# Kernel optimization log

Hardware: AMD Instinct MI355X
Metric: run time of the kernel (lower is better)

## Reference

```python
import jax, jax.numpy as jnp
import numpy as np

B, F, V, E = 4096, 26, 20000, 64
LAYERS = [256, 128, 1]


def setup_inputs() -> dict:
    key = jax.random.key(0)
    ks = jax.random.split(key, 13)
    s = 1.0 / np.sqrt(E)
    inp = {
        "x_idx": jax.random.randint(ks[0], (B, F), 0, V),
        # per-field embedding tables [F, V, E] and linear (bias) tables [F, V, 1]
        "embed_w": jax.random.normal(ks[1], (F, V, E), jnp.float32) * 0.01,
        "embed_b": jax.random.normal(ks[2], (F, V, 1), jnp.float32) * 0.01,
        "attention_w": jax.random.normal(ks[3], (E, E), jnp.float32) * s,
        "attention_b": jax.random.normal(ks[4], (1, E), jnp.float32) * 0.01,
        "attention_p": jax.random.normal(ks[5], (E,), jnp.float32) * 0.01,
        "w0": jax.random.normal(ks[6], (E, LAYERS[0]), jnp.float32) * s,
        "b0": jnp.zeros((LAYERS[0],), jnp.float32),
        "w1": jax.random.normal(ks[7], (LAYERS[0], LAYERS[1]), jnp.float32) * (1.0 / np.sqrt(LAYERS[0])),
        "b1": jnp.zeros((LAYERS[1],), jnp.float32),
        "w2": jax.random.normal(ks[8], (LAYERS[1], LAYERS[2]), jnp.float32) * (1.0 / np.sqrt(LAYERS[1])),
        "b2": jnp.zeros((LAYERS[2],), jnp.float32),
        "bias": jnp.zeros((1,), jnp.float32),
    }
    return inp


def _gather_fields(tables, idx):
    # tables: [F, V, D], idx: [B, F] -> [B, F, D]
    return jax.vmap(lambda tbl, i: tbl[i], in_axes=(0, 1), out_axes=1)(tables, idx)


def reference(x_idx, embed_w, embed_b, attention_w, attention_b, attention_p,
              w0, b0, w1, b1, w2, b2, bias):
    f = embed_w.shape[0]
    xw = _gather_fields(embed_w, x_idx)                      # [B, F, E]
    iu, ju = jnp.triu_indices(f, k=1)                        # P = F*(F-1)/2 pairs, loop order i<j
    pairs = xw[:, iu, :] * xw[:, ju, :]                      # [B, P, E] pairwise FM interactions
    # attention network: relu(pairs @ W + b), score = <p, .>, softmax over pairs
    att_h = jax.nn.relu(jnp.einsum('bpe,ef->bpf', pairs, attention_w) + attention_b)
    scores = jnp.sum(attention_p * att_h, axis=2, keepdims=True)   # [B, P, 1]
    att_out = jax.nn.softmax(scores, axis=1)                       # softmax pooling over pairs
    afm = jnp.sum(att_out * pairs, axis=1)                         # [B, E]
    # MLP head
    h = jax.nn.relu(afm @ w0 + b0)
    h = jax.nn.relu(h @ w1 + b1)
    bilinear = h @ w2 + b2                                         # [B, 1]
    # linear (LR) term from per-field bias tables
    lr = jnp.sum(_gather_fields(embed_b, x_idx), axis=1)           # [B, 1]
    return bilinear + lr + bias
```

## Files before the change

kernel.cpp:

```cpp
#include <hip/hip_runtime.h>
#include <stdint.h>

#define B_N 4096
#define F_N 26
#define V_N 20000
#define E_N 64
#define P_N 325
#define PT  21
#define SPB 8

typedef __attribute__((ext_vector_type(8))) _Float16 half8;
typedef __attribute__((ext_vector_type(4))) _Float16 half4;
typedef __attribute__((ext_vector_type(4))) float floatx4;

__global__ __launch_bounds__(512, 4) void anfm_fused_kernel(
    const int* __restrict__ x_idx, const float* __restrict__ embed_w,
    const float* __restrict__ embed_b, const float* __restrict__ att_w,
    const float* __restrict__ att_b, const float* __restrict__ att_p,
    const float* __restrict__ w0, const float* __restrict__ b0,
    const float* __restrict__ w1, const float* __restrict__ b1,
    const float* __restrict__ w2, const float* __restrict__ b2,
    const float* __restrict__ bias, float* __restrict__ out)
{
    __shared__ _Float16 xwb[SPB][F_N][72];
    __shared__ _Float16 WT[64][72];
    __shared__ unsigned short pijL[336];
    __shared__ float apL[64], abL[64];
    __shared__ _Float16 afmL[16][72];
    __shared__ _Float16 h0L[16][264];
    __shared__ float    h1L[16][132];
    __shared__ float    lrL[SPB];

    const int tid  = threadIdx.x;
    const int lane = tid & 63;
    const int wid  = tid >> 6;
    const int c16  = lane & 15;
    const int g    = lane >> 4;
    const int b    = blockIdx.x * SPB + wid;

    int myidx = (lane < F_N) ? x_idx[b * F_N + lane] : 0;
    float lv  = (lane < F_N) ? embed_b[lane * V_N + myidx] : 0.f;
    float4 gv[7];
    #pragma unroll
    for (int it = 0; it < 7; it++) {
        int f = it * 4 + g;
        int fc = (f < F_N) ? f : 0;
        int idxf = __shfl(myidx, fc);
        const float4* src = reinterpret_cast<const float4*>(
            embed_w + ((size_t)(fc * V_N + idxf)) * E_N);
        gv[it] = src[c16];
    }

    if (tid < 336) {
        int p = tid;
        int i = 0, j = 1;
        if (p < P_N) {
            i = (int)((51.0f - sqrtf(2601.0f - 8.0f * (float)p)) * 0.5f);
            if (i * (51 - i) / 2 > p) i--;
            else if ((i + 1) * (50 - i) / 2 <= p) i++;
            j = p - i * (51 - i) / 2 + i + 1;
        }
        pijL[p] = (unsigned short)((i << 8) | j);
    } else if (tid < 400) {
        apL[tid - 336] = att_p[tid - 336];
    } else if (tid < 464) {
        abL[tid - 400] = att_b[tid - 400];
    }
    for (int z = tid; z < 576; z += 512) {
        int r = z / 72, c = z - r * 72;
        afmL[8 + r][c] = (_Float16)0.f;
    }
    for (int idx = tid; idx < 64 * 64; idx += 512) {
        int k = idx >> 6, col = idx & 63;
        WT[col][k] = (_Float16)att_w[idx];
    }

    #pragma unroll
    for (int it = 0; it < 7; it++) {
        int f = it * 4 + g;
        if (f < F_N) {
            float4 v = gv[it];
            half4 hv = {(_Float16)v.x, (_Float16)v.y, (_Float16)v.z, (_Float16)v.w};
            *reinterpret_cast<half4*>(&xwb[wid][f][c16 * 4]) = hv;
        }
    }
    __syncthreads();

    half8 bfr[4][2];
    #pragma unroll
    for (int nt = 0; nt < 4; nt++)
        #pragma unroll
        for (int s = 0; s < 2; s++)
            bfr[nt][s] = *reinterpret_cast<const half8*>(
                &WT[nt * 16 + c16][s * 32 + g * 8]);

    float acf[16];
    #pragma unroll
    for (int u = 0; u < 16; u++) acf[u] = 0.f;
    float Zp = 0.f;

    #pragma unroll 1
    for (int t = 0; t < PT; t++) {
        int pk = pijL[t * 16 + c16];
        int ri = pk >> 8, rj = pk & 255;
        half8 af[2];
        #pragma unroll
        for (int s = 0; s < 2; s++) {
            half8 xv = *reinterpret_cast<const half8*>(&xwb[wid][ri][s * 32 + g * 8]);
            half8 yv = *reinterpret_cast<const half8*>(&xwb[wid][rj][s * 32 + g * 8]);
            af[s] = xv * yv;
        }
        float scq = 0.f;
        #pragma unroll
        for (int nt = 0; nt < 4; nt++) {
            floatx4 acc = *reinterpret_cast<const floatx4*>(&abL[nt * 16 + g * 4]);
            acc = __builtin_amdgcn_mfma_f32_16x16x32_f16(bfr[nt][0], af[0], acc, 0, 0, 0);
            acc = __builtin_amdgcn_mfma_f32_16x16x32_f16(bfr[nt][1], af[1], acc, 0, 0, 0);
            floatx4 ap4 = *reinterpret_cast<const floatx4*>(&apL[nt * 16 + g * 4]);
            #pragma unroll
            for (int r = 0; r < 4; r++)
                scq = fmaf(ap4[r], fmaxf(acc[r], 0.f), scq);
        }
        scq += __shfl_xor(scq, 16);
        scq += __shfl_xor(scq, 32);
        float w = (t * 16 + c16 < P_N) ? __expf(scq) : 0.f;
        Zp += w;
        #pragma unroll
        for (int s = 0; s < 2; s++)
            #pragma unroll
            for (int u = 0; u < 8; u++)
                acf[s * 8 + u] = fmaf((float)af[s][u], w, acf[s * 8 + u]);
    }

    #pragma unroll
    for (int msk = 1; msk <= 8; msk <<= 1) {
        Zp += __shfl_xor(Zp, msk);
        #pragma unroll
        for (int u = 0; u < 16; u++) acf[u] += __shfl_xor(acf[u], msk);
    }

    if (c16 == 0) {
        float rZ = 1.f / Zp;
        #pragma unroll
        for (int s = 0; s < 2; s++) {
            half4 o0 = {(_Float16)(acf[s * 8 + 0] * rZ), (_Float16)(acf[s * 8 + 1] * rZ),
                        (_Float16)(acf[s * 8 + 2] * rZ), (_Float16)(acf[s * 8 + 3] * rZ)};
            half4 o1 = {(_Float16)(acf[s * 8 + 4] * rZ), (_Float16)(acf[s * 8 + 5] * rZ),
                        (_Float16)(acf[s * 8 + 6] * rZ), (_Float16)(acf[s * 8 + 7] * rZ)};
            *reinterpret_cast<half4*>(&afmL[wid][s * 32 + g * 8])     = o0;
            *reinterpret_cast<half4*>(&afmL[wid][s * 32 + g * 8 + 4]) = o1;
        }
    }
    #pragma unroll
    for (int off = 32; off; off >>= 1) lv += __shfl_xor(lv, off);
    if (lane == 0) lrL[wid] = lv;
    __syncthreads();


    {
        half8 af0[2];
        #pragma unroll
        for (int s = 0; s < 2; s++)
            af0[s] = *reinterpret_cast<const half8*>(&afmL[c16][s * 32 + g * 8]);
        #pragma unroll
        for (int q = 0; q < 2; q++) {
            int n = (wid * 2 + q) * 16 + c16;
            half8 bf[2];
            #pragma unroll
            for (int s = 0; s < 2; s++)
                #pragma unroll
                for (int u = 0; u < 8; u++)
                    bf[s][u] = (_Float16)w0[(s * 32 + g * 8 + u) * 256 + n];
            floatx4 acc = {0.f, 0.f, 0.f, 0.f};
            acc = __builtin_amdgcn_mfma_f32_16x16x32_f16(af0[0], bf[0], acc, 0, 0, 0);
            acc = __builtin_amdgcn_mfma_f32_16x16x32_f16(af0[1], bf[1], acc, 0, 0, 0);
            float b0n = b0[n];
            #pragma unroll
            for (int r = 0; r < 4; r++)
                h0L[g * 4 + r][n] = (_Float16)fmaxf(acc[r] + b0n, 0.f);
        }
    }
    __syncthreads();

    {
        int n = wid * 16 + c16;
        floatx4 acc = {0.f, 0.f, 0.f, 0.f};
        #pragma unroll
        for (int ks = 0; ks < 8; ks++) {
            half8 af1 = *reinterpret_cast<const half8*>(&h0L[c16][ks * 32 + g * 8]);
            half8 bf;
            #pragma unroll
            for (int u = 0; u < 8; u++)
                bf[u] = (_Float16)w1[(ks * 32 + g * 8 + u) * 128 + n];
            acc = __builtin_amdgcn_mfma_f32_16x16x32_f16(af1, bf, acc, 0, 0, 0);
        }
        float b1n = b1[n];
        #pragma unroll
        for (int r = 0; r < 4; r++)
            h1L[g * 4 + r][n] = fmaxf(acc[r] + b1n, 0.f);
    }
    __syncthreads();

    {
        float part = fmaf(h1L[wid][lane * 2], w2[lane * 2],
                          h1L[wid][lane * 2 + 1] * w2[lane * 2 + 1]);
        #pragma unroll
        for (int off = 32; off; off >>= 1) part += __shfl_xor(part, off);
        if (lane == 0)
            out[blockIdx.x * SPB + wid] = part + b2[0] + bias[0] + lrL[wid];
    }
}

extern "C" void kernel_launch(void* const* d_in, const int* in_sizes, int n_in,
                              void* d_out, int out_size, void* d_ws, size_t ws_size,
                              hipStream_t stream) {
    const int*   x_idx   = (const int*)d_in[0];
    const float* embed_w = (const float*)d_in[1];
    const float* embed_b = (const float*)d_in[2];
    const float* att_w   = (const float*)d_in[3];
    const float* att_b   = (const float*)d_in[4];
    const float* att_p   = (const float*)d_in[5];
    const float* w0      = (const float*)d_in[6];
    const float* b0      = (const float*)d_in[7];
    const float* w1      = (const float*)d_in[8];
    const float* b1      = (const float*)d_in[9];
    const float* w2      = (const float*)d_in[10];
    const float* b2      = (const float*)d_in[11];
    const float* bias    = (const float*)d_in[12];
    float*       out     = (float*)d_out;

    anfm_fused_kernel<<<B_N / SPB, 512, 0, stream>>>(
        x_idx, embed_w, embed_b, att_w, att_b, att_p,
        w0, b0, w1, b1, w2, b2, bias, out);
}
```

Baseline: 34.28 us.

## Split each sample's pair loop across two waves, halving samples per block

```diff
diff --git a/kernel.cpp b/kernel.cpp
--- a/kernel.cpp
+++ b/kernel.cpp
@@ -7,7 +7,7 @@
 #define E_N 64
 #define P_N 325
 #define PT  21
-#define SPB 8
+#define SPB 4
 
 typedef __attribute__((ext_vector_type(8))) _Float16 half8;
 typedef __attribute__((ext_vector_type(4))) _Float16 half4;
@@ -26,24 +26,28 @@
     __shared__ _Float16 WT[64][72];
     __shared__ unsigned short pijL[336];
     __shared__ float apL[64], abL[64];
+    __shared__ float afm_part[SPB][2][64];
+    __shared__ float ZpL[SPB][2];
+    __shared__ float lrL[SPB];
     __shared__ _Float16 afmL[16][72];
     __shared__ _Float16 h0L[16][264];
     __shared__ float    h1L[16][132];
-    __shared__ float    lrL[SPB];
 
     const int tid  = threadIdx.x;
     const int lane = tid & 63;
     const int wid  = tid >> 6;
     const int c16  = lane & 15;
     const int g    = lane >> 4;
-    const int b    = blockIdx.x * SPB + wid;
+    const int smp  = wid >> 1;
+    const int wv   = wid & 1;
+    const int b    = blockIdx.x * SPB + smp;
 
     int myidx = (lane < F_N) ? x_idx[b * F_N + lane] : 0;
-    float lv  = (lane < F_N) ? embed_b[lane * V_N + myidx] : 0.f;
-    float4 gv[7];
-    #pragma unroll
-    for (int it = 0; it < 7; it++) {
-        int f = it * 4 + g;
+    float lv  = (wv == 0 && lane < F_N) ? embed_b[lane * V_N + myidx] : 0.f;
+    float4 gv[4];
+    #pragma unroll
+    for (int it = 0; it < 4; it++) {
+        int f = it * 8 + wv * 4 + g;
         int fc = (f < F_N) ? f : 0;
         int idxf = __shfl(myidx, fc);
         const float4* src = reinterpret_cast<const float4*>(
@@ -66,9 +70,9 @@
     } else if (tid < 464) {
         abL[tid - 400] = att_b[tid - 400];
     }
-    for (int z = tid; z < 576; z += 512) {
+    for (int z = tid; z < 864; z += 512) {
         int r = z / 72, c = z - r * 72;
-        afmL[8 + r][c] = (_Float16)0.f;
+        afmL[4 + r][c] = (_Float16)0.f;
     }
     for (int idx = tid; idx < 64 * 64; idx += 512) {
         int k = idx >> 6, col = idx & 63;
@@ -76,12 +80,12 @@
     }
 
     #pragma unroll
-    for (int it = 0; it < 7; it++) {
-        int f = it * 4 + g;
+    for (int it = 0; it < 4; it++) {
+        int f = it * 8 + wv * 4 + g;
         if (f < F_N) {
             float4 v = gv[it];
             half4 hv = {(_Float16)v.x, (_Float16)v.y, (_Float16)v.z, (_Float16)v.w};
-            *reinterpret_cast<half4*>(&xwb[wid][f][c16 * 4]) = hv;
+            *reinterpret_cast<half4*>(&xwb[smp][f][c16 * 4]) = hv;
         }
     }
     __syncthreads();
@@ -100,14 +104,14 @@
     float Zp = 0.f;
 
     #pragma unroll 1
-    for (int t = 0; t < PT; t++) {
+    for (int t = wv; t < PT; t += 2) {
         int pk = pijL[t * 16 + c16];
         int ri = pk >> 8, rj = pk & 255;
         half8 af[2];
         #pragma unroll
         for (int s = 0; s < 2; s++) {
-            half8 xv = *reinterpret_cast<const half8*>(&xwb[wid][ri][s * 32 + g * 8]);
-            half8 yv = *reinterpret_cast<const half8*>(&xwb[wid][rj][s * 32 + g * 8]);
+            half8 xv = *reinterpret_cast<const half8*>(&xwb[smp][ri][s * 32 + g * 8]);
+            half8 yv = *reinterpret_cast<const half8*>(&xwb[smp][rj][s * 32 + g * 8]);
             af[s] = xv * yv;
         }
         float scq = 0.f;
@@ -140,20 +144,25 @@
     }
 
     if (c16 == 0) {
-        float rZ = 1.f / Zp;
-        #pragma unroll
-        for (int s = 0; s < 2; s++) {
-            half4 o0 = {(_Float16)(acf[s * 8 + 0] * rZ), (_Float16)(acf[s * 8 + 1] * rZ),
-                        (_Float16)(acf[s * 8 + 2] * rZ), (_Float16)(acf[s * 8 + 3] * rZ)};
-            half4 o1 = {(_Float16)(acf[s * 8 + 4] * rZ), (_Float16)(acf[s * 8 + 5] * rZ),
-                        (_Float16)(acf[s * 8 + 6] * rZ), (_Float16)(acf[s * 8 + 7] * rZ)};
-            *reinterpret_cast<half4*>(&afmL[wid][s * 32 + g * 8])     = o0;
-            *reinterpret_cast<half4*>(&afmL[wid][s * 32 + g * 8 + 4]) = o1;
-        }
-    }
-    #pragma unroll
-    for (int off = 32; off; off >>= 1) lv += __shfl_xor(lv, off);
-    if (lane == 0) lrL[wid] = lv;
+        #pragma unroll
+        for (int s = 0; s < 2; s++)
+            #pragma unroll
+            for (int u = 0; u < 8; u++)
+                afm_part[smp][wv][s * 32 + g * 8 + u] = acf[s * 8 + u];
+        if (g == 0) ZpL[smp][wv] = Zp;
+    }
+    if (wv == 0) {
+        #pragma unroll
+        for (int off = 32; off; off >>= 1) lv += __shfl_xor(lv, off);
+        if (lane == 0) lrL[smp] = lv;
+    }
+    __syncthreads();
+
+    if (tid < SPB * 64) {
+        int s = tid >> 6, e = tid & 63;
+        float rz = 1.f / (ZpL[s][0] + ZpL[s][1]);
+        afmL[s][e] = (_Float16)((afm_part[s][0][e] + afm_part[s][1][e]) * rz);
+    }
     __syncthreads();
 
 
@@ -201,7 +210,7 @@
     }
     __syncthreads();
 
-    {
+    if (wid < SPB) {
         float part = fmaf(h1L[wid][lane * 2], w2[lane * 2],
                           h1L[wid][lane * 2 + 1] * w2[lane * 2 + 1]);
         #pragma unroll
```

After: 39.01 us. 1.14x slower.
